# Performance work log

Hardware: AMD Instinct MI355X
Metric: run time of the kernel (lower is better)

The kernel has to match this reference:

```python
import jax, jax.numpy as jnp
import numpy as np

D_MODEL = 1024
N_HEADS = 16
D_K = D_MODEL // N_HEADS
SCALE = 1.0 / np.sqrt(D_K).astype(np.float32)
NEG = -1000000000.0


def setup_inputs() -> dict:
    key = jax.random.key(0)
    ks = jax.random.split(key, 5)
    B, S = 2, 2048
    query = jax.random.normal(ks[0], (B, S, D_MODEL), dtype=jnp.float32)
    k_in = jax.random.normal(ks[1], (B, S, D_MODEL), dtype=jnp.float32)
    v_in = jax.random.normal(ks[2], (B, S, D_MODEL), dtype=jnp.float32)
    # causal mask, broadcast over batch and heads; 0 entries get -1e9
    mask = jnp.tril(jnp.ones((S, S), dtype=jnp.int32))[None, None, :, :]
    w_qkv = jax.random.normal(ks[3], (D_MODEL, 3 * D_MODEL), dtype=jnp.float32) * (1.0 / np.sqrt(D_MODEL))
    w_o = jax.random.normal(ks[4], (D_MODEL, D_MODEL), dtype=jnp.float32) * (1.0 / np.sqrt(D_MODEL))
    return {"query": query, "key": k_in, "value": v_in, "mask": mask, "w_qkv": w_qkv, "w_o": w_o}


def reference(query, key, value, mask, w_qkv, w_o):
    # NOTE: original module ignores `key`/`value`; q,k,v all come from `query`.
    B, S, _ = query.shape
    qkv = query @ w_qkv                       # [B,S,3D]
    q, k, v = jnp.split(qkv, 3, axis=-1)
    def heads(x):
        return x.reshape(B, S, N_HEADS, D_K).transpose(0, 2, 1, 3)  # [B,H,S,dk]
    Q, K, V = heads(q), heads(k), heads(v)
    scores = jnp.einsum('bhqd,bhkd->bhqk', Q, K) * SCALE            # [B,H,S,S]
    scores = jnp.where(mask == 0, NEG, scores)
    attn = jax.nn.softmax(scores, axis=-1)
    # Dropout(0.1) treated as eval-mode identity for a deterministic reference.
    context = jnp.einsum('bhqk,bhkd->bhqd', attn, V)                # [B,H,S,dk]
    context = context.transpose(0, 2, 1, 3).reshape(B, S, D_MODEL)
    return context @ w_o
```

## Files before the change

kernel.cpp:

```cpp
#include <hip/hip_runtime.h>
#include <stdint.h>
#include <type_traits>


typedef __attribute__((ext_vector_type(8))) short bf16x8;
typedef __attribute__((ext_vector_type(4))) float f32x4;

#define LOG2E 1.44269504088896340736f
#define QSCALE (0.125f * LOG2E)

__device__ __forceinline__ unsigned short f2b(float f) {
  union { float f; unsigned int i; } x; x.f = f;
  unsigned int i = x.i;
  return (unsigned short)((i + 0x7FFFu + ((i >> 16) & 1u)) >> 16);
}

__device__ __forceinline__ void async16(const void* g, void* l) {
  __builtin_amdgcn_global_load_lds(
      (__attribute__((address_space(1))) void*)g,
      (__attribute__((address_space(3))) void*)l, 16, 0, 0);
}

__device__ __forceinline__ f32x4 mfma16(bf16x8 a, bf16x8 b, f32x4 c) {
  return __builtin_amdgcn_mfma_f32_16x16x32_bf16(a, b, c, 0, 0, 0);
}

__device__ __forceinline__ unsigned int fbits(float f) {
  union { float f; unsigned int i; } x; x.f = f;
  return x.i;
}

__global__ __launch_bounds__(256) void cvt_x(const float* __restrict__ src,
                                             unsigned short* __restrict__ dst) {
  const size_t i = ((size_t)blockIdx.x * 256 + threadIdx.x) * 8;
  float4 a = *(const float4*)(src + i);
  float4 b = *(const float4*)(src + i + 4);
  unsigned short e[8];
  e[0] = f2b(a.x); e[1] = f2b(a.y); e[2] = f2b(a.z); e[3] = f2b(a.w);
  e[4] = f2b(b.x); e[5] = f2b(b.y); e[6] = f2b(b.z); e[7] = f2b(b.w);
  *(uint4*)(dst + i) = *(const uint4*)e;
}

__global__ __launch_bounds__(256) void transpose_cvt(
    const float* __restrict__ src, unsigned short* __restrict__ dst, int R,
    int Ccols, int scale_cols, float scale) {
  __shared__ __align__(16) unsigned short Lt[64 * 64];
  const int r0 = blockIdx.x * 64, c0 = blockIdx.y * 64;
  const float s = (c0 < scale_cols) ? scale : 1.0f;
  const int t = threadIdx.x;
#pragma unroll
  for (int it = 0; it < 4; ++it) {
    int c = it * 256 + t;
    int sr = c >> 4, co = (c & 15) * 4;
    float4 v = *(const float4*)(src + (size_t)(r0 + sr) * Ccols + c0 + co);
    Lt[(co + 0) * 64 + sr] = f2b(v.x * s);
    Lt[(co + 1) * 64 + sr] = f2b(v.y * s);
    Lt[(co + 2) * 64 + sr] = f2b(v.z * s);
    Lt[(co + 3) * 64 + sr] = f2b(v.w * s);
  }
  __syncthreads();
#pragma unroll
  for (int it = 0; it < 2; ++it) {
    int c = it * 256 + t;
    int dr = c >> 3, so = (c & 7) * 8;
    *(uint4*)(dst + (size_t)(c0 + dr) * R + r0 + so) =
        *(const uint4*)(Lt + dr * 64 + so);
  }
}

template <typename CT>
__global__ __launch_bounds__(256) void gemm_bt(
    const unsigned short* __restrict__ A, const unsigned short* __restrict__ Bt,
    CT* __restrict__ C, int M, int N, int K) {
  __shared__ __align__(16) unsigned short As[128 * 32];
  __shared__ __align__(16) unsigned short Bs[128 * 32];
  const int t = threadIdx.x;
  const int w = t >> 6, l = t & 63;
  const int m0 = blockIdx.y * 128, n0 = blockIdx.x * 128;
  const int wm = (w >> 1) * 64, wn = (w & 1) * 64;
  const int lrow = l & 15, lk = (l >> 4) * 8;

  f32x4 acc[4][4] = {};

  for (int k0 = 0; k0 < K; k0 += 32) {
    __syncthreads();
#pragma unroll
    for (int r = 0; r < 2; ++r) {
      const int c = r * 256 + t;
      async16(A + (size_t)(m0 + (c >> 2)) * K + k0 + (c & 3) * 8,
              As + (size_t)(r * 256 + w * 64) * 8);
      async16(Bt + (size_t)(n0 + (c >> 2)) * K + k0 + (c & 3) * 8,
              Bs + (size_t)(r * 256 + w * 64) * 8);
    }
    asm volatile("s_waitcnt vmcnt(0)" ::: "memory");
    __syncthreads();

    bf16x8 af[4], bf[4];
#pragma unroll
    for (int i = 0; i < 4; ++i)
      af[i] = *(const bf16x8*)(As + (wm + i * 16 + lrow) * 32 + lk);
#pragma unroll
    for (int j = 0; j < 4; ++j)
      bf[j] = *(const bf16x8*)(Bs + (wn + j * 16 + lrow) * 32 + lk);
#pragma unroll
    for (int i = 0; i < 4; ++i)
#pragma unroll
      for (int j = 0; j < 4; ++j)
        acc[i][j] = mfma16(af[i], bf[j], acc[i][j]);
  }

#pragma unroll
  for (int i = 0; i < 4; ++i)
#pragma unroll
    for (int j = 0; j < 4; ++j)
#pragma unroll
      for (int r = 0; r < 4; ++r) {
        int gr = m0 + wm + i * 16 + (l >> 4) * 4 + r;
        int gc = n0 + wn + j * 16 + (l & 15);
        if constexpr (std::is_same<CT, unsigned short>::value)
          C[(size_t)gr * N + gc] = f2b(acc[i][j][r]);
        else
          C[(size_t)gr * N + gc] = acc[i][j][r];
      }
}

__global__ __launch_bounds__(256) void gemm_o(
    const unsigned short* __restrict__ A, const unsigned short* __restrict__ Bt,
    float* __restrict__ C, int M, int N, int K) {
  __shared__ __align__(16) unsigned short As[64 * 32];
  __shared__ __align__(16) unsigned short Bs[128 * 32];
  const int t = threadIdx.x;
  const int w = t >> 6, l = t & 63;
  const int m0 = blockIdx.y * 64, n0 = blockIdx.x * 128;
  const int wm = (w & 1) * 32, wn = (w >> 1) * 64;
  const int lrow = l & 15, lk = (l >> 4) * 8;

  f32x4 acc[2][4] = {};

  for (int k0 = 0; k0 < K; k0 += 32) {
    __syncthreads();
    async16(A + (size_t)(m0 + (t >> 2)) * K + k0 + (t & 3) * 8,
            As + (size_t)(w * 64) * 8);
#pragma unroll
    for (int r = 0; r < 2; ++r) {
      const int c = r * 256 + t;
      async16(Bt + (size_t)(n0 + (c >> 2)) * K + k0 + (c & 3) * 8,
              Bs + (size_t)(r * 256 + w * 64) * 8);
    }
    asm volatile("s_waitcnt vmcnt(0)" ::: "memory");
    __syncthreads();

    bf16x8 af[2], bf[4];
#pragma unroll
    for (int i = 0; i < 2; ++i)
      af[i] = *(const bf16x8*)(As + (wm + i * 16 + lrow) * 32 + lk);
#pragma unroll
    for (int j = 0; j < 4; ++j)
      bf[j] = *(const bf16x8*)(Bs + (wn + j * 16 + lrow) * 32 + lk);
#pragma unroll
    for (int i = 0; i < 2; ++i)
#pragma unroll
      for (int j = 0; j < 4; ++j)
        acc[i][j] = mfma16(af[i], bf[j], acc[i][j]);
  }

#pragma unroll
  for (int i = 0; i < 2; ++i)
#pragma unroll
    for (int j = 0; j < 4; ++j)
#pragma unroll
      for (int r = 0; r < 4; ++r) {
        int gr = m0 + wm + i * 16 + (l >> 4) * 4 + r;
        int gc = n0 + wn + j * 16 + (l & 15);
        C[(size_t)gr * N + gc] = acc[i][j][r];
      }
}

__global__ __launch_bounds__(256) void v_relayout(
    const unsigned short* __restrict__ qkv, unsigned short* __restrict__ Vt) {
  __shared__ __align__(16) unsigned short Lt[64 * 64];
  const int s0 = blockIdx.x * 64;
  const int bh = blockIdx.y;
  const int b = bh >> 4, h = bh & 15;
  const int t = threadIdx.x;
#pragma unroll
  for (int r = 0; r < 2; ++r) {
    int c = r * 256 + t;
    int sr = c >> 3, doff = (c & 7) * 8;
    uint4 v = *(const uint4*)(qkv + (size_t)(b * 2048 + s0 + sr) * 3072 + 2048 +
                              h * 64 + doff);
    const unsigned short* e = (const unsigned short*)&v;
#pragma unroll
    for (int j = 0; j < 8; ++j) Lt[(doff + j) * 64 + sr] = e[j];
  }
  __syncthreads();
#pragma unroll
  for (int r = 0; r < 2; ++r) {
    int c = r * 256 + t;
    int dr = c >> 3, so = (c & 7) * 8;
    *(uint4*)(Vt + ((size_t)bh * 64 + dr) * 2048 + s0 + so) =
        *(const uint4*)(Lt + dr * 64 + so);
  }
}

__global__ __launch_bounds__(512, 4) void attn_fwd(
    const unsigned short* __restrict__ qkv,
    const unsigned short* __restrict__ Vt,
    unsigned short* __restrict__ ctx) {
  __shared__ __align__(16) unsigned short Ks[2][64 * 64];
  __shared__ __align__(16) unsigned short Vs[2][64 * 64];
  __shared__ __align__(16) unsigned short Ps[8][16 * 72];

  const int ti = blockIdx.x;
  const int bh = blockIdx.y;
  const int b = bh >> 4, h = bh & 15;
  const int t = threadIdx.x;
  const int g = t >> 8;
  const int tl = t & 255;
  const int w = tl >> 6;
  const int gw = t >> 6;
  const int l = t & 63;
  const int lm = l & 15, lq = l >> 4;
  const int sw = lm & 7;
  const int c0 = (lq ^ sw) * 8;
  const int c1 = ((lq + 4) ^ sw) * 8;

  const int qt0[2] = {ti * 64, (31 - ti) * 64};
  const int ktmax = 31 - ti;
  const int nsup = (ktmax >> 1) + 1;

  const unsigned short* Qp = qkv + (size_t)(b * 2048) * 3072 + h * 64;
  const unsigned short* Kp = qkv + (size_t)(b * 2048) * 3072 + 1024 + h * 64;
  const unsigned short* Vb = Vt + (size_t)bh * 64 * 2048;

  bf16x8 qf[2][2];
#pragma unroll
  for (int qt = 0; qt < 2; ++qt) {
    const int qrow = qt0[qt] + w * 16 + lm;
    qf[qt][0] = *(const bf16x8*)(Qp + (size_t)qrow * 3072 + lq * 8);
    qf[qt][1] = *(const bf16x8*)(Qp + (size_t)qrow * 3072 + 32 + lq * 8);
  }

  f32x4 oacc[2][4] = {};
  float lsum[2] = {0.f, 0.f};

  for (int jj = 0; jj < nsup; ++jj) {
    const int kt = 2 * jj + g;
    const bool have = (kt <= ktmax);
    __syncthreads();
    if (have) {
      const int kk0 = kt * 64;
#pragma unroll
      for (int r = 0; r < 2; ++r) {
        int cl = r * 256 + tl;
        int row = cl >> 3, cp = cl & 7;
        int so = ((cp ^ (row & 7)) * 8);
        async16(Kp + (size_t)(kk0 + row) * 3072 + so,
                Ks[g] + (size_t)(r * 256 + w * 64) * 8);
        async16(Vb + (size_t)row * 2048 + kk0 + so,
                Vs[g] + (size_t)(r * 256 + w * 64) * 8);
      }
    }
    asm volatile("s_waitcnt vmcnt(0)" ::: "memory");
    __syncthreads();
    if (!have) continue;

    const unsigned short* Kc = Ks[g];
    const unsigned short* Vc = Vs[g];

    bf16x8 vf[8];
#pragma unroll
    for (int nt = 0; nt < 4; ++nt) {
      const unsigned short* vr = Vc + (nt * 16 + lm) * 64;
      vf[nt] = *(const bf16x8*)(vr + c0);
      vf[4 + nt] = *(const bf16x8*)(vr + c1);
    }

#pragma unroll
    for (int qt = 0; qt < 2; ++qt) {
      if (qt == 0 && kt > ti) continue;
      f32x4 sacc[4] = {};
#pragma unroll
      for (int mt = 0; mt < 4; ++mt) {
        const unsigned short* kr = Kc + (mt * 16 + lm) * 64;
        bf16x8 bk0 = *(const bf16x8*)(kr + c0);
        bf16x8 bk1 = *(const bf16x8*)(kr + c1);
        sacc[mt] = mfma16(bk0, qf[qt][0], sacc[mt]);
        sacc[mt] = mfma16(bk1, qf[qt][1], sacc[mt]);
      }

      const bool diag = (kt == ((qt == 0) ? ti : ktmax));
      const int qloc = w * 16 + lm;
#pragma unroll
      for (int mt = 0; mt < 4; ++mt) {
        float p0 = __builtin_amdgcn_exp2f(sacc[mt][0]);
        float p1 = __builtin_amdgcn_exp2f(sacc[mt][1]);
        float p2 = __builtin_amdgcn_exp2f(sacc[mt][2]);
        float p3 = __builtin_amdgcn_exp2f(sacc[mt][3]);
        if (diag) {
          const int kvb = mt * 16 + lq * 4;
          if (kvb + 0 > qloc) p0 = 0.f;
          if (kvb + 1 > qloc) p1 = 0.f;
          if (kvb + 2 > qloc) p2 = 0.f;
          if (kvb + 3 > qloc) p3 = 0.f;
        }
        lsum[qt] += (p0 + p1) + (p2 + p3);
        uint2 pk;
        pk.x = (fbits(p1) & 0xFFFF0000u) | (fbits(p0) >> 16);
        pk.y = (fbits(p3) & 0xFFFF0000u) | (fbits(p2) >> 16);
        *(uint2*)(&Ps[gw][lm * 72 + mt * 16 + lq * 4]) = pk;
      }
      asm volatile("s_waitcnt lgkmcnt(0)" ::: "memory");

#pragma unroll
      for (int ks = 0; ks < 2; ++ks) {
        bf16x8 pa = *(const bf16x8*)(&Ps[gw][lm * 72 + ks * 32 + lq * 8]);
#pragma unroll
        for (int nt = 0; nt < 4; ++nt)
          oacc[qt][nt] = mfma16(pa, vf[ks * 4 + nt], oacc[qt][nt]);
      }
    }
  }

#pragma unroll
  for (int qt = 0; qt < 2; ++qt) {
    lsum[qt] += __shfl_xor(lsum[qt], 16, 64);
    lsum[qt] += __shfl_xor(lsum[qt], 32, 64);
  }

  __syncthreads();
  float* fbuf[2] = {(float*)Ks, (float*)Vs};
  float* lbuf = (float*)Ps;
  if (g == 1) {
#pragma unroll
    for (int qt = 0; qt < 2; ++qt) {
#pragma unroll
      for (int nt = 0; nt < 4; ++nt)
#pragma unroll
        for (int r = 0; r < 4; ++r)
          fbuf[qt][(w * 16 + lq * 4 + r) * 64 + nt * 16 + lm] = oacc[qt][nt][r];
      if (l < 16) lbuf[qt * 64 + w * 16 + lm] = lsum[qt];
    }
  }
  __syncthreads();
  if (g == 0) {
#pragma unroll
    for (int qt = 0; qt < 2; ++qt) {
      const float ltot = lsum[qt] + lbuf[qt * 64 + w * 16 + lm];
      float rinv[4];
#pragma unroll
      for (int r = 0; r < 4; ++r)
        rinv[r] = 1.f / __shfl(ltot, lq * 4 + r, 64);
#pragma unroll
      for (int nt = 0; nt < 4; ++nt)
#pragma unroll
        for (int r = 0; r < 4; ++r) {
          float v = oacc[qt][nt][r] +
                    fbuf[qt][(w * 16 + lq * 4 + r) * 64 + nt * 16 + lm];
          size_t tok = (size_t)b * 2048 + qt0[qt] + w * 16 + lq * 4 + r;
          ctx[tok * 1024 + h * 64 + nt * 16 + lm] = f2b(v * rinv[r]);
        }
    }
  }
}

extern "C" void kernel_launch(void* const* d_in, const int* in_sizes, int n_in,
                              void* d_out, int out_size, void* d_ws,
                              size_t ws_size, hipStream_t stream) {
  const float* query = (const float*)d_in[0];
  const float* w_qkv = (const float*)d_in[4];
  const float* w_o = (const float*)d_in[5];
  float* out = (float*)d_out;

  unsigned short* ws = (unsigned short*)d_ws;
  unsigned short* wqkvT = ws;
  unsigned short* woT = wqkvT + (size_t)3072 * 1024;
  unsigned short* Xb = woT + (size_t)1024 * 1024;
  unsigned short* qkv = Xb + (size_t)4096 * 1024;
  unsigned short* Vt = qkv + (size_t)4096 * 3072;
  unsigned short* ctx = Xb;

  cvt_x<<<dim3(2048), 256, 0, stream>>>(query, Xb);
  transpose_cvt<<<dim3(16, 48), 256, 0, stream>>>(w_qkv, wqkvT, 1024, 3072,
                                                  1024, QSCALE);
  transpose_cvt<<<dim3(16, 16), 256, 0, stream>>>(w_o, woT, 1024, 1024, 0,
                                                  1.0f);
  gemm_bt<unsigned short><<<dim3(24, 32), 256, 0, stream>>>(Xb, wqkvT, qkv,
                                                            4096, 3072, 1024);
  v_relayout<<<dim3(32, 32), 256, 0, stream>>>(qkv, Vt);
  attn_fwd<<<dim3(16, 32), 512, 0, stream>>>(qkv, Vt, ctx);
  gemm_o<<<dim3(8, 64), 256, 0, stream>>>(ctx, woT, out, 4096, 1024, 1024);
}
```

Before: 218.0 us.

## Merge prep kernels, fuse V transpose into QKV GEMM, use K=64 swizzled tiles

The three conversion/transpose launches become one prep kernel that dispatches on block index. The QKV GEMM now writes V blocks transposed through LDS straight into Vt, so the separate v_relayout kernel is gone. Both GEMMs now stage 64-wide K tiles with an XOR swizzle on the LDS layout, which halves the number of barriers and is meant to avoid bank conflicts. The larger tiles raise LDS use per block, which may lower occupancy.

```diff
diff --git a/kernel.cpp b/kernel.cpp
--- a/kernel.cpp
+++ b/kernel.cpp
@@ -1,6 +1,5 @@
 #include <hip/hip_runtime.h>
 #include <stdint.h>
-#include <type_traits>
 
 
 typedef __attribute__((ext_vector_type(8))) short bf16x8;
@@ -30,24 +29,30 @@
   return x.i;
 }
 
-__global__ __launch_bounds__(256) void cvt_x(const float* __restrict__ src,
-                                             unsigned short* __restrict__ dst) {
-  const size_t i = ((size_t)blockIdx.x * 256 + threadIdx.x) * 8;
-  float4 a = *(const float4*)(src + i);
-  float4 b = *(const float4*)(src + i + 4);
-  unsigned short e[8];
-  e[0] = f2b(a.x); e[1] = f2b(a.y); e[2] = f2b(a.z); e[3] = f2b(a.w);
-  e[4] = f2b(b.x); e[5] = f2b(b.y); e[6] = f2b(b.z); e[7] = f2b(b.w);
-  *(uint4*)(dst + i) = *(const uint4*)e;
-}
-
-__global__ __launch_bounds__(256) void transpose_cvt(
-    const float* __restrict__ src, unsigned short* __restrict__ dst, int R,
-    int Ccols, int scale_cols, float scale) {
+__global__ __launch_bounds__(256) void prep(
+    const float* __restrict__ X, const float* __restrict__ Wqkv,
+    const float* __restrict__ Wo, unsigned short* __restrict__ Xb,
+    unsigned short* __restrict__ WqkvT, unsigned short* __restrict__ WoT) {
   __shared__ __align__(16) unsigned short Lt[64 * 64];
-  const int r0 = blockIdx.x * 64, c0 = blockIdx.y * 64;
-  const float s = (c0 < scale_cols) ? scale : 1.0f;
+  const int bx = blockIdx.x;
   const int t = threadIdx.x;
+  if (bx < 2048) {
+    const size_t i = ((size_t)bx * 256 + t) * 8;
+    float4 a = *(const float4*)(X + i);
+    float4 b = *(const float4*)(X + i + 4);
+    unsigned short e[8];
+    e[0] = f2b(a.x); e[1] = f2b(a.y); e[2] = f2b(a.z); e[3] = f2b(a.w);
+    e[4] = f2b(b.x); e[5] = f2b(b.y); e[6] = f2b(b.z); e[7] = f2b(b.w);
+    *(uint4*)(Xb + i) = *(const uint4*)e;
+    return;
+  }
+  const bool is_qkv = (bx < 2816);
+  const int bid = is_qkv ? bx - 2048 : bx - 2816;
+  const float* src = is_qkv ? Wqkv : Wo;
+  unsigned short* dst = is_qkv ? WqkvT : WoT;
+  const int Ccols = is_qkv ? 3072 : 1024;
+  const int r0 = (bid & 15) * 64, c0 = (bid >> 4) * 64;
+  const float s = (is_qkv && c0 < 1024) ? QSCALE : 1.0f;
 #pragma unroll
   for (int it = 0; it < 4; ++it) {
     int c = it * 256 + t;
@@ -63,144 +68,165 @@
   for (int it = 0; it < 2; ++it) {
     int c = it * 256 + t;
     int dr = c >> 3, so = (c & 7) * 8;
-    *(uint4*)(dst + (size_t)(c0 + dr) * R + r0 + so) =
+    *(uint4*)(dst + (size_t)(c0 + dr) * 1024 + r0 + so) =
         *(const uint4*)(Lt + dr * 64 + so);
   }
 }
 
-template <typename CT>
-__global__ __launch_bounds__(256) void gemm_bt(
+__global__ __launch_bounds__(256) void gemm_qkv(
     const unsigned short* __restrict__ A, const unsigned short* __restrict__ Bt,
-    CT* __restrict__ C, int M, int N, int K) {
-  __shared__ __align__(16) unsigned short As[128 * 32];
-  __shared__ __align__(16) unsigned short Bs[128 * 32];
+    unsigned short* __restrict__ C, unsigned short* __restrict__ Vt) {
+  constexpr int K = 1024, N = 3072;
+  __shared__ __align__(16) unsigned short Sm[16896];
+  unsigned short* As = Sm;
+  unsigned short* Bs = Sm + 8192;
+  unsigned short* Lt = Sm;
+
   const int t = threadIdx.x;
   const int w = t >> 6, l = t & 63;
   const int m0 = blockIdx.y * 128, n0 = blockIdx.x * 128;
   const int wm = (w >> 1) * 64, wn = (w & 1) * 64;
-  const int lrow = l & 15, lk = (l >> 4) * 8;
+  const int lrow = l & 15, lq = l >> 4;
 
   f32x4 acc[4][4] = {};
 
-  for (int k0 = 0; k0 < K; k0 += 32) {
-    __syncthreads();
-#pragma unroll
-    for (int r = 0; r < 2; ++r) {
+  for (int k0 = 0; k0 < K; k0 += 64) {
+    __syncthreads();
+#pragma unroll
+    for (int r = 0; r < 4; ++r) {
       const int c = r * 256 + t;
-      async16(A + (size_t)(m0 + (c >> 2)) * K + k0 + (c & 3) * 8,
-              As + (size_t)(r * 256 + w * 64) * 8);
-      async16(Bt + (size_t)(n0 + (c >> 2)) * K + k0 + (c & 3) * 8,
-              Bs + (size_t)(r * 256 + w * 64) * 8);
+      const int row = c >> 3;
+      const int so = ((c & 7) ^ (row & 7)) * 8;
+      async16(A + (size_t)(m0 + row) * K + k0 + so,
+              As + (size_t)(r * 256 + t) * 8);
+      async16(Bt + (size_t)(n0 + row) * K + k0 + so,
+              Bs + (size_t)(r * 256 + t) * 8);
     }
     asm volatile("s_waitcnt vmcnt(0)" ::: "memory");
     __syncthreads();
 
-    bf16x8 af[4], bf[4];
+#pragma unroll
+    for (int kh = 0; kh < 2; ++kh) {
+      bf16x8 af[4], bf[4];
+      const int phys = ((kh * 4 + lq) ^ (lrow & 7)) * 8;
+#pragma unroll
+      for (int i = 0; i < 4; ++i)
+        af[i] = *(const bf16x8*)(As + (wm + i * 16 + lrow) * 64 + phys);
+#pragma unroll
+      for (int j = 0; j < 4; ++j)
+        bf[j] = *(const bf16x8*)(Bs + (wn + j * 16 + lrow) * 64 + phys);
+#pragma unroll
+      for (int i = 0; i < 4; ++i)
+#pragma unroll
+        for (int j = 0; j < 4; ++j)
+          acc[i][j] = mfma16(af[i], bf[j], acc[i][j]);
+    }
+  }
+
+  if (n0 < 2048) {
 #pragma unroll
     for (int i = 0; i < 4; ++i)
-      af[i] = *(const bf16x8*)(As + (wm + i * 16 + lrow) * 32 + lk);
-#pragma unroll
-    for (int j = 0; j < 4; ++j)
-      bf[j] = *(const bf16x8*)(Bs + (wn + j * 16 + lrow) * 32 + lk);
+#pragma unroll
+      for (int j = 0; j < 4; ++j)
+#pragma unroll
+        for (int r = 0; r < 4; ++r) {
+          int gr = m0 + wm + i * 16 + lq * 4 + r;
+          int gc = n0 + wn + j * 16 + lrow;
+          C[(size_t)gr * N + gc] = f2b(acc[i][j][r]);
+        }
+  } else {
+    __syncthreads();
 #pragma unroll
     for (int i = 0; i < 4; ++i)
 #pragma unroll
-      for (int j = 0; j < 4; ++j)
-        acc[i][j] = mfma16(af[i], bf[j], acc[i][j]);
-  }
-
-#pragma unroll
-  for (int i = 0; i < 4; ++i)
-#pragma unroll
-    for (int j = 0; j < 4; ++j)
-#pragma unroll
-      for (int r = 0; r < 4; ++r) {
-        int gr = m0 + wm + i * 16 + (l >> 4) * 4 + r;
-        int gc = n0 + wn + j * 16 + (l & 15);
-        if constexpr (std::is_same<CT, unsigned short>::value)
-          C[(size_t)gr * N + gc] = f2b(acc[i][j][r]);
-        else
-          C[(size_t)gr * N + gc] = acc[i][j][r];
-      }
+      for (int j = 0; j < 4; ++j) {
+        int col_loc = wn + j * 16 + lrow;
+        int row_loc = wm + i * 16 + lq * 4;
+        uint2 pk;
+        pk.x = (unsigned int)f2b(acc[i][j][0]) |
+               ((unsigned int)f2b(acc[i][j][1]) << 16);
+        pk.y = (unsigned int)f2b(acc[i][j][2]) |
+               ((unsigned int)f2b(acc[i][j][3]) << 16);
+        *(uint2*)(Lt + col_loc * 132 + row_loc) = pk;
+      }
+    __syncthreads();
+    const int b = m0 >> 11, s0 = m0 & 2047;
+    const int vb0 = n0 - 2048;
+#pragma unroll
+    for (int rnd = 0; rnd < 8; ++rnd) {
+      int vrow = rnd * 16 + (t >> 4);
+      int sloc = (t & 15) * 8;
+      int vcol = vb0 + vrow;
+      int bh = b * 16 + (vcol >> 6);
+      int d = vcol & 63;
+      *(uint4*)(Vt + ((size_t)bh * 64 + d) * 2048 + s0 + sloc) =
+          *(const uint4*)(Lt + vrow * 132 + sloc);
+    }
+  }
 }
 
 __global__ __launch_bounds__(256) void gemm_o(
     const unsigned short* __restrict__ A, const unsigned short* __restrict__ Bt,
     float* __restrict__ C, int M, int N, int K) {
-  __shared__ __align__(16) unsigned short As[64 * 32];
-  __shared__ __align__(16) unsigned short Bs[128 * 32];
+  __shared__ __align__(16) unsigned short As[64 * 64];
+  __shared__ __align__(16) unsigned short Bs[128 * 64];
   const int t = threadIdx.x;
   const int w = t >> 6, l = t & 63;
   const int m0 = blockIdx.y * 64, n0 = blockIdx.x * 128;
   const int wm = (w & 1) * 32, wn = (w >> 1) * 64;
-  const int lrow = l & 15, lk = (l >> 4) * 8;
+  const int lrow = l & 15, lq = l >> 4;
 
   f32x4 acc[2][4] = {};
 
-  for (int k0 = 0; k0 < K; k0 += 32) {
-    __syncthreads();
-    async16(A + (size_t)(m0 + (t >> 2)) * K + k0 + (t & 3) * 8,
-            As + (size_t)(w * 64) * 8);
+  for (int k0 = 0; k0 < K; k0 += 64) {
+    __syncthreads();
 #pragma unroll
     for (int r = 0; r < 2; ++r) {
       const int c = r * 256 + t;
-      async16(Bt + (size_t)(n0 + (c >> 2)) * K + k0 + (c & 3) * 8,
-              Bs + (size_t)(r * 256 + w * 64) * 8);
+      const int row = c >> 3;
+      const int so = ((c & 7) ^ (row & 7)) * 8;
+      async16(A + (size_t)(m0 + row) * K + k0 + so,
+              As + (size_t)(r * 256 + t) * 8);
+    }
+#pragma unroll
+    for (int r = 0; r < 4; ++r) {
+      const int c = r * 256 + t;
+      const int row = c >> 3;
+      const int so = ((c & 7) ^ (row & 7)) * 8;
+      async16(Bt + (size_t)(n0 + row) * K + k0 + so,
+              Bs + (size_t)(r * 256 + t) * 8);
     }
     asm volatile("s_waitcnt vmcnt(0)" ::: "memory");
     __syncthreads();
 
-    bf16x8 af[2], bf[4];
-#pragma unroll
-    for (int i = 0; i < 2; ++i)
-      af[i] = *(const bf16x8*)(As + (wm + i * 16 + lrow) * 32 + lk);
+#pragma unroll
+    for (int kh = 0; kh < 2; ++kh) {
+      bf16x8 af[2], bf[4];
+      const int phys = ((kh * 4 + lq) ^ (lrow & 7)) * 8;
+#pragma unroll
+      for (int i = 0; i < 2; ++i)
+        af[i] = *(const bf16x8*)(As + (wm + i * 16 + lrow) * 64 + phys);
+#pragma unroll
+      for (int j = 0; j < 4; ++j)
+        bf[j] = *(const bf16x8*)(Bs + (wn + j * 16 + lrow) * 64 + phys);
+#pragma unroll
+      for (int i = 0; i < 2; ++i)
+#pragma unroll
+        for (int j = 0; j < 4; ++j)
+          acc[i][j] = mfma16(af[i], bf[j], acc[i][j]);
+    }
+  }
+
+#pragma unroll
+  for (int i = 0; i < 2; ++i)
 #pragma unroll
     for (int j = 0; j < 4; ++j)
-      bf[j] = *(const bf16x8*)(Bs + (wn + j * 16 + lrow) * 32 + lk);
-#pragma unroll
-    for (int i = 0; i < 2; ++i)
-#pragma unroll
-      for (int j = 0; j < 4; ++j)
-        acc[i][j] = mfma16(af[i], bf[j], acc[i][j]);
-  }
-
-#pragma unroll
-  for (int i = 0; i < 2; ++i)
-#pragma unroll
-    for (int j = 0; j < 4; ++j)
 #pragma unroll
       for (int r = 0; r < 4; ++r) {
-        int gr = m0 + wm + i * 16 + (l >> 4) * 4 + r;
-        int gc = n0 + wn + j * 16 + (l & 15);
+        int gr = m0 + wm + i * 16 + lq * 4 + r;
+        int gc = n0 + wn + j * 16 + lrow;
         C[(size_t)gr * N + gc] = acc[i][j][r];
       }
-}
-
-__global__ __launch_bounds__(256) void v_relayout(
-    const unsigned short* __restrict__ qkv, unsigned short* __restrict__ Vt) {
-  __shared__ __align__(16) unsigned short Lt[64 * 64];
-  const int s0 = blockIdx.x * 64;
-  const int bh = blockIdx.y;
-  const int b = bh >> 4, h = bh & 15;
-  const int t = threadIdx.x;
-#pragma unroll
-  for (int r = 0; r < 2; ++r) {
-    int c = r * 256 + t;
-    int sr = c >> 3, doff = (c & 7) * 8;
-    uint4 v = *(const uint4*)(qkv + (size_t)(b * 2048 + s0 + sr) * 3072 + 2048 +
-                              h * 64 + doff);
-    const unsigned short* e = (const unsigned short*)&v;
-#pragma unroll
-    for (int j = 0; j < 8; ++j) Lt[(doff + j) * 64 + sr] = e[j];
-  }
-  __syncthreads();
-#pragma unroll
-  for (int r = 0; r < 2; ++r) {
-    int c = r * 256 + t;
-    int dr = c >> 3, so = (c & 7) * 8;
-    *(uint4*)(Vt + ((size_t)bh * 64 + dr) * 2048 + s0 + so) =
-        *(const uint4*)(Lt + dr * 64 + so);
-  }
 }
 
 __global__ __launch_bounds__(512, 4) void attn_fwd(
@@ -380,14 +406,8 @@
   unsigned short* Vt = qkv + (size_t)4096 * 3072;
   unsigned short* ctx = Xb;
 
-  cvt_x<<<dim3(2048), 256, 0, stream>>>(query, Xb);
-  transpose_cvt<<<dim3(16, 48), 256, 0, stream>>>(w_qkv, wqkvT, 1024, 3072,
-                                                  1024, QSCALE);
-  transpose_cvt<<<dim3(16, 16), 256, 0, stream>>>(w_o, woT, 1024, 1024, 0,
-                                                  1.0f);
-  gemm_bt<unsigned short><<<dim3(24, 32), 256, 0, stream>>>(Xb, wqkvT, qkv,
-                                                            4096, 3072, 1024);
-  v_relayout<<<dim3(32, 32), 256, 0, stream>>>(qkv, Vt);
+  prep<<<dim3(3072), 256, 0, stream>>>(query, w_qkv, w_o, Xb, wqkvT, woT);
+  gemm_qkv<<<dim3(24, 32), 256, 0, stream>>>(Xb, wqkvT, qkv, Vt);
   attn_fwd<<<dim3(16, 32), 512, 0, stream>>>(qkv, Vt, ctx);
   gemm_o<<<dim3(8, 64), 256, 0, stream>>>(ctx, woT, out, 4096, 1024, 1024);
 }
```

Result: faster. 205.3 us (-5.8%).
